# Kernel tuning notes

Hardware: AMD Instinct MI355X
Metric: run time of the kernel (lower is better)

Reference implementation:

```python
import jax, jax.numpy as jnp
import numpy as np

HID = 512; HH = HID // 2; INP = 1; OUT = 1
INH = int(HID * 0.3); EXC = HID - INH            # 153 / 359
N = 3 * HH + 2 * HID + INP                       # 1793 total units
ALM_EXC_START = 3 * HH + HID                      # start of ALM excitatory block
T_CONST = 0.1; SIGMA_REC = 0.01
B, T = 128, 300


def _np_masks():
    rng = np.random.default_rng(0)
    n_zeros = int(np.ceil(0.9 * HH))
    sparse = np.ones((HH, HH), np.float32)
    for c in range(HH):
        sparse[rng.permutation(HH)[:n_zeros], c] = 0.0
    alm2str = np.concatenate([np.ones((HH, EXC), np.float32), np.zeros((HH, INH), np.float32)], 1)
    thal2d1 = np.concatenate([np.ones((HH // 2, HID), np.float32), np.zeros((HH // 2, HID), np.float32)], 0)
    alm2d1 = 1.0 - thal2d1
    iti2d1 = np.concatenate([np.ones((HH // 2, INP), np.float32), np.zeros((HH // 2, INP), np.float32)], 0)
    alm_sign = np.concatenate([np.ones(EXC, np.float32), -np.ones(INH, np.float32)])  # alm2alm_D diagonal
    return sparse, alm2str, thal2d1, alm2d1, iti2d1, alm_sign

_SPARSE, _ALM2STR, _THAL2D1M, _ALM2D1M, _ITI2D1M, _ALMSIGN = [jnp.asarray(a) for a in _np_masks()]


def _clip(w):
    return jnp.clip(w, 1e-10, 1.0)               # F.hardtanh(w, 1e-10, 1)


def _build_W(d12d1_w, d12d2_w, d22d1_w, d22d2_w, d22stn_w, d12thal_w, stn2thal_w,
             thal2alm_w, alm2alm_w, thal2d1_w, thal2d2_w, alm2d1_w, alm2d2_w,
             inp_w_d1, inp_w_d2):
    z_ss = jnp.zeros((HH, HH)); z_sl = jnp.zeros((HH, HID))
    z_ls = jnp.zeros((HID, HH)); z_ll = jnp.zeros((HID, HID))
    z_si = jnp.zeros((HH, INP)); z_li = jnp.zeros((HID, INP))
    # striatal recurrence: sparse_mask * hardtanh(w) @ (-I)
    d12d1 = -(_SPARSE * _clip(d12d1_w)); d12d2 = -(_SPARSE * _clip(d12d2_w))
    d22d1 = -(_SPARSE * _clip(d22d1_w)); d22d2 = -(_SPARSE * _clip(d22d2_w))
    row_d1 = jnp.concatenate([d12d1, d22d1, z_ss, _THAL2D1M * _clip(thal2d1_w),
                              _ALM2D1M * _ALM2STR * _clip(alm2d1_w), _ITI2D1M * _clip(inp_w_d1)], 1)
    row_d2 = jnp.concatenate([d12d2, d22d2, z_ss, _clip(thal2d2_w),
                              _ALM2STR * _clip(alm2d2_w), _clip(inp_w_d2)], 1)
    row_stn = jnp.concatenate([z_ss, _clip(d22stn_w), z_ss, z_sl, z_sl, z_si], 1)
    row_thal = jnp.concatenate([_clip(d12thal_w), z_ls, -_clip(stn2thal_w), z_ll, z_ll, z_li], 1)  # stn2thal @ (-I)
    row_alm = jnp.concatenate([z_ls, z_ls, z_ls, _clip(thal2alm_w),
                               _clip(alm2alm_w) * _ALMSIGN[None, :], z_li], 1)      # alm2alm @ D (Dale)
    row_iti = jnp.zeros((INP, N))
    return jnp.concatenate([row_d1, row_d2, row_stn, row_thal, row_alm, row_iti], 0)


def setup_inputs() -> dict:
    key = jax.random.key(0)
    ks = jax.random.split(key, 24)
    u = lambda k, s: jax.random.uniform(k, s, jnp.float32) * 0.01   # uniform(0, 0.01) init
    return {
        "inp": jax.random.uniform(ks[0], (B, T, INP), jnp.float32),
        "cue_inp": jax.random.uniform(ks[1], (B, T, INP), jnp.float32),
        "inhib_stim": jnp.zeros((B, T, N), jnp.float32),
        "hn": jax.random.uniform(ks[2], (1, B, N), jnp.float32),
        "xn": jax.random.uniform(ks[3], (1, B, N), jnp.float32),
        "noise": jax.random.normal(ks[4], (B, T, N), jnp.float32),
        "d12d1_w": u(ks[5], (HH, HH)), "d12d2_w": u(ks[6], (HH, HH)),
        "d22d1_w": u(ks[7], (HH, HH)), "d22d2_w": u(ks[8], (HH, HH)),
        "d22stn_w": u(ks[9], (HH, HH)), "d12thal_w": u(ks[10], (HID, HH)),
        "stn2thal_w": u(ks[11], (HID, HH)), "thal2alm_w": u(ks[12], (HID, HID)),
        "alm2alm_w": u(ks[13], (HID, HID)), "thal2d1_w": u(ks[14], (HH, HID)),
        "thal2d2_w": u(ks[15], (HH, HID)), "alm2d1_w": u(ks[16], (HH, HID)),
        "alm2d2_w": u(ks[17], (HH, HID)), "inp_w_d1": u(ks[18], (HH, INP)),
        "inp_w_d2": u(ks[19], (HH, INP)), "out_w_alm": u(ks[20], (OUT, EXC)),
    }


def reference(inp, cue_inp, inhib_stim, hn, xn, noise,
              d12d1_w, d12d2_w, d22d1_w, d22d2_w, d22stn_w, d12thal_w, stn2thal_w,
              thal2alm_w, alm2alm_w, thal2d1_w, thal2d2_w, alm2d1_w, alm2d2_w,
              inp_w_d1, inp_w_d2, out_w_alm):
    W = _build_W(d12d1_w, d12d2_w, d22d1_w, d22d2_w, d22stn_w, d12thal_w, stn2thal_w,
                 thal2alm_w, alm2alm_w, thal2d1_w, thal2d2_w, alm2d1_w, alm2d2_w,
                 inp_w_d1, inp_w_d2)
    # tonic current: 0.1 everywhere except ITI units
    tonic = jnp.concatenate([0.1 * jnp.ones(N - INP, jnp.float32), jnp.zeros(INP, jnp.float32)])
    seq = (inhib_stim.swapaxes(0, 1),                 # [T, B, N]
           (inp + cue_inp).swapaxes(0, 1),            # [T, B, INP] -> injected into ITI units
           noise.swapaxes(0, 1))                      # [T, B, N]

    def step(carry, s):
        x, h = carry
        inh_t, iti_t, noise_t = s
        drive = h @ W.T + tonic + inh_t + SIGMA_REC * noise_t
        drive = drive.at[:, N - INP:].add(iti_t)
        x = x + T_CONST * (-x + drive)
        h = jax.nn.relu(x)
        out = h[:, ALM_EXC_START:ALM_EXC_START + EXC] @ out_w_alm.T
        return (x, h), (h, x, out)

    (_, _), (hs, xs, outs) = jax.lax.scan(step, (xn[0], hn[0]), seq)
    return hs.swapaxes(0, 1), xs.swapaxes(0, 1), outs.swapaxes(0, 1)
```

## Files before the change

kernel.cpp:

```cpp
#include <hip/hip_runtime.h>
#include <stdint.h>
#include <string.h>

#define NREAL 1793
#define NPAD  1824
#define NROWP 1808
#define WSTR  1832
#define NBLK  113
#define NGRP  2
#define TSTEPS 300
#define BATCH 128
#define XS_OFF 68851200
#define OUT_OFF 137702400
#define LOFF (16 * WSTR)
#define LOSCALE 4096.0f
#define LOINV  2.44140625e-4f

#define ARR_IDX(g,s)  (((g) * 8 + (s)) * 32)
#define MID_IDX(g)    ((16 + (g)) * 32)
#define FLAG_IDX(g,s) ((18 + (g) * 8 + (s)) * 32)
#define STRIPE_SZ(s)  ((s) == 0 ? 15u : 14u)

typedef _Float16 half_t;
typedef __attribute__((ext_vector_type(8))) _Float16 half8;
typedef __attribute__((ext_vector_type(4))) float f32x4;
typedef __attribute__((ext_vector_type(4))) unsigned int uint4v;

__device__ __forceinline__ float clipw(float w) {
  return fminf(fmaxf(w, 1e-10f), 1.0f);
}

__device__ __forceinline__ void store_pack_llc(uint32_t* p, uint32_t v) {
  asm volatile("global_store_dword %0, %1, off sc0 sc1"
               :: "v"((unsigned long long)(uintptr_t)p), "v"(v)
               : "memory");
}

__global__ __launch_bounds__(256)
void build_w(const float* __restrict__ d12d1, const float* __restrict__ d12d2,
             const float* __restrict__ d22d1, const float* __restrict__ d22d2,
             const float* __restrict__ d22stn, const float* __restrict__ d12thal,
             const float* __restrict__ stn2thal, const float* __restrict__ thal2alm,
             const float* __restrict__ alm2alm, const float* __restrict__ thal2d1,
             const float* __restrict__ thal2d2, const float* __restrict__ alm2d1,
             const float* __restrict__ alm2d2, const float* __restrict__ inpw1,
             const float* __restrict__ inpw2, const unsigned int* __restrict__ mbits,
             half_t* __restrict__ W)
{
  int idx = blockIdx.x * 256 + threadIdx.x;
  if (idx >= NROWP * NPAD) return;
  int i = idx / NPAD, j = idx - (idx / NPAD) * NPAD;
  float v = 0.f;
  if (i < NREAL && j < NREAL) {
    if (i < 256) {
      if (j < 512) {
        int jj = j & 255;
        unsigned bit = (mbits[(i << 3) + (jj >> 5)] >> (jj & 31)) & 1u;
        float wv = (j < 256) ? d12d1[(i << 8) + jj] : d22d1[(i << 8) + jj];
        v = bit ? -clipw(wv) : 0.f;
      } else if (j < 768) {
      } else if (j < 1280) {
        if (i < 128) v = clipw(thal2d1[(i << 9) + (j - 768)]);
      } else if (j < 1792) {
        int jj = j - 1280;
        if (i >= 128 && jj < 359) v = clipw(alm2d1[(i << 9) + jj]);
      } else {
        if (i < 128) v = clipw(inpw1[i]);
      }
    } else if (i < 512) {
      int ii = i - 256;
      if (j < 512) {
        int jj = j & 255;
        unsigned bit = (mbits[(ii << 3) + (jj >> 5)] >> (jj & 31)) & 1u;
        float wv = (j < 256) ? d12d2[(ii << 8) + jj] : d22d2[(ii << 8) + jj];
        v = bit ? -clipw(wv) : 0.f;
      } else if (j < 768) {
      } else if (j < 1280) {
        v = clipw(thal2d2[(ii << 9) + (j - 768)]);
      } else if (j < 1792) {
        int jj = j - 1280;
        if (jj < 359) v = clipw(alm2d2[(ii << 9) + jj]);
      } else {
        v = clipw(inpw2[ii]);
      }
    } else if (i < 768) {
      int ii = i - 512;
      if (j >= 256 && j < 512) v = clipw(d22stn[(ii << 8) + (j - 256)]);
    } else if (i < 1280) {
      int ii = i - 768;
      if (j < 256) v = clipw(d12thal[(ii << 8) + j]);
      else if (j >= 512 && j < 768) v = -clipw(stn2thal[(ii << 8) + (j - 512)]);
    } else if (i < 1792) {
      int ii = i - 1280;
      if (j >= 768 && j < 1280) v = clipw(thal2alm[(ii << 9) + (j - 768)]);
      else if (j >= 1280) {
        int jj = j - 1280;
        v = clipw(alm2alm[(ii << 9) + jj]) * ((jj < 359) ? 1.f : -1.f);
      }
    }
  }
  half_t vh = (half_t)v;
  half_t vl = (half_t)((v - (float)vh) * LOSCALE);
  W[idx] = vh;
  W[(size_t)NROWP * NPAD + idx] = vl;
}

__global__ __launch_bounds__(256)
void init_h(const float* __restrict__ hn, uint32_t* __restrict__ hbuf)
{
  const size_t P4 = (size_t)BATCH * NPAD;
  int idx = blockIdx.x * 256 + threadIdx.x;
  if (idx >= BATCH * NPAD) return;
  int b = idx / NPAD, k = idx - b * NPAD;
  float v = (k < NREAL) ? hn[b * NREAL + k] : 0.f;
  half_t vh = (half_t)v;
  half_t vl = (half_t)((v - (float)vh) * LOSCALE);
  uint32_t hp = (uint32_t)(*(unsigned short*)&vh) |
                ((uint32_t)(*(unsigned short*)&vl) << 16);
  hbuf[idx]      = hp;
  hbuf[P4 + idx] = 0u;
}

__global__ __launch_bounds__(256)
void rnn_step_all(const half_t* __restrict__ Wg, uint32_t* __restrict__ hbuf,
                  unsigned int* __restrict__ cnt,
                  const float* __restrict__ inp, const float* __restrict__ cue,
                  const float* __restrict__ inhib, const float* __restrict__ noise,
                  const float* __restrict__ xn, const float* __restrict__ outw,
                  float* __restrict__ dout)
{
  __shared__ __align__(16) half_t Wl[2 * 16 * WSTR];
  const int tid = threadIdx.x;
  const int bid = blockIdx.x;
  const int g  = bid / NBLK;
  const int nb = bid - g * NBLK;
  const int r0 = nb * 16;
  const int bg = g * 64;
  const size_t P4 = (size_t)BATCH * NPAD;

  const int lane = tid & 63;
  const int w    = tid >> 6;
  const int n_i  = lane & 15;
  const int kq   = lane >> 4;
  const int row  = r0 + n_i;
  const bool valid = row < NREAL;
  const int b0 = bg + 16 * w + kq * 4;
  const int bA = bg + 16 * w + n_i;
  const int wl_b = n_i * WSTR + kq * 8;

  float inh[4], noi[4];
  #pragma unroll
  for (int r = 0; r < 4; ++r) {
    inh[r] = 0.f; noi[r] = 0.f;
    if (valid) {
      int ei = ((b0 + r) * TSTEPS) * NREAL + row;
      inh[r] = __builtin_nontemporal_load(&inhib[ei]);
      noi[r] = __builtin_nontemporal_load(&noise[ei]);
    }
  }

  for (int idx = tid; idx < 2 * 16 * (NPAD / 8); idx += 256) {
    int p   = idx / (16 * (NPAD / 8));
    int rem = idx - p * 16 * (NPAD / 8);
    int rr  = rem / (NPAD / 8);
    int cc  = (rem - rr * (NPAD / 8)) * 8;
    *(uint4v*)&Wl[p * LOFF + rr * WSTR + cc] =
        *(const uint4v*)&Wg[(size_t)p * NROWP * NPAD + (size_t)(r0 + rr) * NPAD + cc];
  }
  __syncthreads();

  int lo0=0,hi0=0,lo1=0,hi1=0,lo2=0,hi2=0;
  if (r0 < 128)       { lo0=0;  hi0=16; lo1=24; hi1=40; lo2=56; hi2=57; }
  else if (r0 < 256)  { lo0=0;  hi0=16; lo1=40; hi1=52; }
  else if (r0 < 512)  { lo0=0;  hi0=16; lo1=24; hi1=52; lo2=56; hi2=57; }
  else if (r0 < 768)  { lo0=8;  hi0=16; }
  else if (r0 < 1280) { lo0=0;  hi0=8;  lo1=16; hi1=24; }
  else if (r0 < 1792) { lo0=24; hi0=56; }

  float xr[4];
  #pragma unroll
  for (int r = 0; r < 4; ++r)
    xr[r] = valid ? xn[(size_t)(b0 + r) * NREAL + row] : 0.f;

  const float wout = (valid && row >= 1280 && row < 1639) ? outw[row - 1280] : 0.f;
  const float tonic = (valid && row < 1792) ? 0.1f : 0.f;
  const bool is_iti = (row == 1792);
  const bool do_out = (r0 >= 1280 && r0 < 1639);

  #pragma unroll 1
  for (int t = 0; t < TSTEPS; ++t) {
    const uint32_t* hr = hbuf + (size_t)(t & 1) * P4;
    uint32_t*       hw = hbuf + (size_t)((t & 1) ^ 1) * P4;

    float itv[4];
    #pragma unroll
    for (int r = 0; r < 4; ++r) {
      int bt = (b0 + r) * TSTEPS + t;
      itv[r] = is_iti ? (inp[bt] + cue[bt]) : 0.f;
    }

    const uint32_t* ap = hr + (size_t)bA * NPAD + kq * 8;
    f32x4 acc0 = {0.f, 0.f, 0.f, 0.f};
    f32x4 acc1 = {0.f, 0.f, 0.f, 0.f};
    f32x4 acc2 = {0.f, 0.f, 0.f, 0.f};

#define DO_CHUNK(kc) { \
      uint4v q0 = *(const uint4v*)(ap + (kc) * 32); \
      uint4v q1 = *(const uint4v*)(ap + (kc) * 32 + 4); \
      uint4v uh, ul; \
      uh.x = __builtin_amdgcn_perm(q0.y, q0.x, 0x05040100u); \
      uh.y = __builtin_amdgcn_perm(q0.w, q0.z, 0x05040100u); \
      uh.z = __builtin_amdgcn_perm(q1.y, q1.x, 0x05040100u); \
      uh.w = __builtin_amdgcn_perm(q1.w, q1.z, 0x05040100u); \
      ul.x = __builtin_amdgcn_perm(q0.y, q0.x, 0x07060302u); \
      ul.y = __builtin_amdgcn_perm(q0.w, q0.z, 0x07060302u); \
      ul.z = __builtin_amdgcn_perm(q1.y, q1.x, 0x07060302u); \
      ul.w = __builtin_amdgcn_perm(q1.w, q1.z, 0x07060302u); \
      union { uint4v u; half8 h; } ch, cl; \
      ch.u = uh; cl.u = ul; \
      half8 bvh = *(const half8*)&Wl[wl_b + (kc) * 32]; \
      half8 bvl = *(const half8*)&Wl[LOFF + wl_b + (kc) * 32]; \
      acc0 = __builtin_amdgcn_mfma_f32_16x16x32_f16(ch.h, bvh, acc0, 0, 0, 0); \
      acc1 = __builtin_amdgcn_mfma_f32_16x16x32_f16(ch.h, bvl, acc1, 0, 0, 0); \
      acc2 = __builtin_amdgcn_mfma_f32_16x16x32_f16(cl.h, bvh, acc2, 0, 0, 0); }

    #pragma unroll 8
    for (int kc = lo0; kc < hi0; ++kc) DO_CHUNK(kc)
    #pragma unroll 8
    for (int kc = lo1; kc < hi1; ++kc) DO_CHUNK(kc)
    #pragma unroll 8
    for (int kc = lo2; kc < hi2; ++kc) DO_CHUNK(kc)
#undef DO_CHUNK

    float op[4];
    #pragma unroll
    for (int r = 0; r < 4; ++r) {
      float drive = acc0[r] + LOINV * (acc1[r] + acc2[r])
                    + tonic + inh[r] + 0.01f * noi[r] + itv[r];
      float xv = xr[r] + 0.1f * (drive - xr[r]);
      float hv = fmaxf(xv, 0.f);
      xr[r] = xv;
      int bt = (b0 + r) * TSTEPS + t;
      if (valid) {
        int ei = bt * NREAL + row;
        __builtin_nontemporal_store(hv, &dout[ei]);
        __builtin_nontemporal_store(xv, &dout[XS_OFF + ei]);
      }
      half_t hh = (half_t)hv;
      half_t hl = (half_t)((hv - (float)hh) * LOSCALE);
      uint32_t hp = (uint32_t)(*(unsigned short*)&hh) |
                    ((uint32_t)(*(unsigned short*)&hl) << 16);
      store_pack_llc(&hw[(size_t)(b0 + r) * NPAD + row], hp);
      op[r] = hv * wout;
    }

    if (do_out) {
      #pragma unroll
      for (int r = 0; r < 4; ++r) {
        float v = op[r];
        v += __shfl_xor(v, 1); v += __shfl_xor(v, 2);
        v += __shfl_xor(v, 4); v += __shfl_xor(v, 8);
        if (n_i == 0) atomicAdd(&dout[OUT_OFF + (b0 + r) * TSTEPS + t], v);
      }
    }

    if (t + 1 < TSTEPS) {
      #pragma unroll
      for (int r = 0; r < 4; ++r) {
        if (valid) {
          int ei = ((b0 + r) * TSTEPS + (t + 1)) * NREAL + row;
          inh[r] = __builtin_nontemporal_load(&inhib[ei]);
          noi[r] = __builtin_nontemporal_load(&noise[ei]);
        }
      }
      asm volatile("s_waitcnt vmcnt(8)" ::: "memory");
      __builtin_amdgcn_s_barrier();
      if (tid == 0) {
        const int s = nb & 7;
        const unsigned epoch = (unsigned)(t + 1);
        unsigned old = atomicAdd(&cnt[ARR_IDX(g, s)], 1u);
        if (old == epoch * STRIPE_SZ(s) - 1u) {
          unsigned mo = atomicAdd(&cnt[MID_IDX(g)], 1u);
          if (mo == epoch * 8u - 1u) {
            #pragma unroll
            for (int f = 0; f < 8; ++f)
              __hip_atomic_store(&cnt[FLAG_IDX(g, f)], epoch,
                                 __ATOMIC_RELAXED, __HIP_MEMORY_SCOPE_AGENT);
          }
        }
        int spins = 0;
        while (__hip_atomic_load(&cnt[FLAG_IDX(g, s)], __ATOMIC_RELAXED,
                                 __HIP_MEMORY_SCOPE_AGENT) < epoch) {
          if (spins < 4) {
            __builtin_amdgcn_s_sleep(1);
          } else {
            __builtin_amdgcn_s_sleep(8);
          }
          ++spins;
        }
        __builtin_amdgcn_fence(__ATOMIC_ACQUIRE, "agent");
      }
      __builtin_amdgcn_s_barrier();
    }
  }
}

static void compute_sparse_mask(uint32_t* mb) {
  uint32_t pool[4];
  uint32_t hc = 0x43b0d7e5u;
  auto hashmix = [&hc](uint32_t value) -> uint32_t {
    value ^= hc; hc *= 0x931e8875u; value *= hc; value ^= value >> 16; return value;
  };
  auto mixf = [](uint32_t x, uint32_t y) -> uint32_t {
    uint32_t r = x * 0xca01f9ddu;
    r -= y * 0x4973f715u;
    r ^= r >> 16;
    return r;
  };
  for (int i = 0; i < 4; ++i) pool[i] = hashmix(0u);
  for (int s = 0; s < 4; ++s)
    for (int d = 0; d < 4; ++d)
      if (s != d) pool[d] = mixf(pool[d], hashmix(pool[s]));
  uint32_t st[8];
  uint32_t hb = 0x8b51f9ddu;
  for (int i = 0; i < 8; ++i) {
    uint32_t dv = pool[i & 3];
    dv ^= hb; hb *= 0x58f38dedu; dv *= hb; dv ^= dv >> 16;
    st[i] = dv;
  }
  uint64_t v64[4];
  for (int i = 0; i < 4; ++i) v64[i] = (uint64_t)st[2 * i] | ((uint64_t)st[2 * i + 1] << 32);
  typedef unsigned __int128 u128;
  const u128 MULT = ((u128)0x2360ed051fc65da4ULL << 64) | 0x4385df649fccf645ULL;
  u128 initstate = ((u128)v64[0] << 64) | v64[1];
  u128 initseq   = ((u128)v64[2] << 64) | v64[3];
  u128 state = 0, inc = (initseq << 1) | 1;
  state = state * MULT + inc;
  state += initstate;
  state = state * MULT + inc;
  bool has32 = false; uint32_t cached = 0;
  auto next64 = [&]() -> uint64_t {
    state = state * MULT + inc;
    uint64_t hi = (uint64_t)(state >> 64), lo = (uint64_t)state;
    unsigned rot = (unsigned)(state >> 122);
    uint64_t x = hi ^ lo;
    return (x >> rot) | (x << ((64 - rot) & 63));
  };
  auto next32 = [&]() -> uint32_t {
    if (has32) { has32 = false; return cached; }
    uint64_t v = next64();
    has32 = true; cached = (uint32_t)(v >> 32);
    return (uint32_t)v;
  };
  auto rinterval = [&](uint32_t mx) -> uint32_t {
    if (mx == 0) return 0;
    uint32_t mask = mx;
    mask |= mask >> 1; mask |= mask >> 2; mask |= mask >> 4;
    mask |= mask >> 8; mask |= mask >> 16;
    uint32_t value;
    do { value = next32() & mask; } while (value > mx);
    return value;
  };
  for (int i = 0; i < 256 * 8; ++i) mb[i] = 0xFFFFFFFFu;
  int perm[256];
  for (int c = 0; c < 256; ++c) {
    for (int i = 0; i < 256; ++i) perm[i] = i;
    for (int i = 255; i >= 1; --i) {
      uint32_t j = rinterval((uint32_t)i);
      int tmp = perm[i]; perm[i] = perm[j]; perm[j] = tmp;
    }
    for (int z = 0; z < 231; ++z)
      mb[perm[z] * 8 + (c >> 5)] &= ~(1u << (c & 31));
  }
}

extern "C" void kernel_launch(void* const* d_in, const int* in_sizes, int n_in,
                              void* d_out, int out_size, void* d_ws, size_t ws_size,
                              hipStream_t stream)
{
  (void)in_sizes; (void)n_in; (void)out_size; (void)ws_size;
  const float* inp   = (const float*)d_in[0];
  const float* cue   = (const float*)d_in[1];
  const float* inhib = (const float*)d_in[2];
  const float* hn    = (const float*)d_in[3];
  const float* xn    = (const float*)d_in[4];
  const float* noise = (const float*)d_in[5];
  const float* outw  = (const float*)d_in[21];
  float* dout = (float*)d_out;

  char* ws = (char*)d_ws;
  const size_t W_BYTES = (size_t)2 * NROWP * NPAD * sizeof(half_t);
  const size_t H_BYTES = (size_t)2 * BATCH * NPAD * 4;
  half_t*   W    = (half_t*)ws;
  uint32_t* hbuf = (uint32_t*)(ws + W_BYTES);
  unsigned int* mbits = (unsigned int*)(ws + W_BYTES + H_BYTES);
  unsigned int* cnt   = (unsigned int*)(ws + W_BYTES + H_BYTES + 8192);

  static uint32_t hmask[256 * 8];
  compute_sparse_mask(hmask);
  (void)hipMemcpyAsync(mbits, hmask, sizeof(hmask), hipMemcpyHostToDevice, stream);
  (void)hipMemsetAsync(cnt, 0, 8192, stream);
  (void)hipMemsetAsync((char*)d_out + (size_t)OUT_OFF * 4, 0, 38400 * 4, stream);

  build_w<<<(NROWP * NPAD + 255) / 256, 256, 0, stream>>>(
      (const float*)d_in[6],  (const float*)d_in[7],  (const float*)d_in[8],
      (const float*)d_in[9],  (const float*)d_in[10], (const float*)d_in[11],
      (const float*)d_in[12], (const float*)d_in[13], (const float*)d_in[14],
      (const float*)d_in[15], (const float*)d_in[16], (const float*)d_in[17],
      (const float*)d_in[18], (const float*)d_in[19], (const float*)d_in[20],
      mbits, W);
  init_h<<<(BATCH * NPAD + 255) / 256, 256, 0, stream>>>(hn, hbuf);

  void* args[] = {(void*)&W, (void*)&hbuf, (void*)&cnt, (void*)&inp, (void*)&cue,
                  (void*)&inhib, (void*)&noise, (void*)&xn, (void*)&outw, (void*)&dout};
  hipError_t err = hipLaunchCooperativeKernel(reinterpret_cast<void*>(rnn_step_all),
                                              dim3(NGRP * NBLK), dim3(256), args, 0, stream);
  if (err != hipSuccess) {
    rnn_step_all<<<dim3(NGRP * NBLK), dim3(256), 0, stream>>>(
        W, hbuf, cnt, inp, cue, inhib, noise, xn, outw, dout);
  }
}
```

Measured before the change: 4.808 ms.

## Move output projection to a single block one step late and batch h loads

```diff
diff --git a/kernel.cpp b/kernel.cpp
--- a/kernel.cpp
+++ b/kernel.cpp
@@ -34,6 +34,54 @@
   asm volatile("global_store_dword %0, %1, off sc0 sc1"
                :: "v"((unsigned long long)(uintptr_t)p), "v"(v)
                : "memory");
+}
+
+__device__ __forceinline__ float unpack_h(uint32_t p) {
+  unsigned short uh = (unsigned short)(p & 0xffffu);
+  unsigned short ul = (unsigned short)(p >> 16);
+  half_t hh = *(half_t*)&uh;
+  half_t hl = *(half_t*)&ul;
+  return (float)hh + LOINV * (float)hl;
+}
+
+template<int LO0, int N0, int LO1, int N1, int LO2, int N2>
+__device__ __forceinline__ void seg_mfma(const uint32_t* __restrict__ ap,
+                                         const half_t* __restrict__ Wl, int wl_b,
+                                         f32x4& acc0, f32x4& acc1, f32x4& acc2)
+{
+  constexpr int NC = N0 + N1 + N2;
+  if (NC == 0) return;
+  uint4v q0[NC ? NC : 1], q1[NC ? NC : 1];
+  #pragma unroll
+  for (int i = 0; i < NC; ++i) {
+    const int kc = (i < N0) ? (LO0 + i)
+                 : (i < N0 + N1) ? (LO1 + i - N0)
+                 : (LO2 + i - N0 - N1);
+    q0[i] = *(const uint4v*)(ap + kc * 32);
+    q1[i] = *(const uint4v*)(ap + kc * 32 + 4);
+  }
+  #pragma unroll
+  for (int i = 0; i < NC; ++i) {
+    const int kc = (i < N0) ? (LO0 + i)
+                 : (i < N0 + N1) ? (LO1 + i - N0)
+                 : (LO2 + i - N0 - N1);
+    uint4v uh, ul;
+    uh.x = __builtin_amdgcn_perm(q0[i].y, q0[i].x, 0x05040100u);
+    uh.y = __builtin_amdgcn_perm(q0[i].w, q0[i].z, 0x05040100u);
+    uh.z = __builtin_amdgcn_perm(q1[i].y, q1[i].x, 0x05040100u);
+    uh.w = __builtin_amdgcn_perm(q1[i].w, q1[i].z, 0x05040100u);
+    ul.x = __builtin_amdgcn_perm(q0[i].y, q0[i].x, 0x07060302u);
+    ul.y = __builtin_amdgcn_perm(q0[i].w, q0[i].z, 0x07060302u);
+    ul.z = __builtin_amdgcn_perm(q1[i].y, q1[i].x, 0x07060302u);
+    ul.w = __builtin_amdgcn_perm(q1[i].w, q1[i].z, 0x07060302u);
+    union { uint4v u; half8 h; } ch, cl;
+    ch.u = uh; cl.u = ul;
+    half8 bvh = *(const half8*)&Wl[wl_b + kc * 32];
+    half8 bvl = *(const half8*)&Wl[LOFF + wl_b + kc * 32];
+    acc0 = __builtin_amdgcn_mfma_f32_16x16x32_f16(ch.h, bvh, acc0, 0, 0, 0);
+    acc1 = __builtin_amdgcn_mfma_f32_16x16x32_f16(ch.h, bvl, acc1, 0, 0, 0);
+    acc2 = __builtin_amdgcn_mfma_f32_16x16x32_f16(cl.h, bvh, acc2, 0, 0, 0);
+  }
 }
 
 __global__ __launch_bounds__(256)
@@ -121,7 +169,7 @@
   hbuf[P4 + idx] = 0u;
 }
 
-__global__ __launch_bounds__(256)
+__global__ __launch_bounds__(256, 1)
 void rnn_step_all(const half_t* __restrict__ Wg, uint32_t* __restrict__ hbuf,
                   unsigned int* __restrict__ cnt,
                   const float* __restrict__ inp, const float* __restrict__ cue,
@@ -147,6 +195,7 @@
   const int b0 = bg + 16 * w + kq * 4;
   const int bA = bg + 16 * w + n_i;
   const int wl_b = n_i * WSTR + kq * 8;
+  const bool is_outblk = (r0 == 512);
 
   float inh[4], noi[4];
   #pragma unroll
@@ -169,23 +218,18 @@
   }
   __syncthreads();
 
-  int lo0=0,hi0=0,lo1=0,hi1=0,lo2=0,hi2=0;
-  if (r0 < 128)       { lo0=0;  hi0=16; lo1=24; hi1=40; lo2=56; hi2=57; }
-  else if (r0 < 256)  { lo0=0;  hi0=16; lo1=40; hi1=52; }
-  else if (r0 < 512)  { lo0=0;  hi0=16; lo1=24; hi1=52; lo2=56; hi2=57; }
-  else if (r0 < 768)  { lo0=8;  hi0=16; }
-  else if (r0 < 1280) { lo0=0;  hi0=8;  lo1=16; hi1=24; }
-  else if (r0 < 1792) { lo0=24; hi0=56; }
-
   float xr[4];
   #pragma unroll
   for (int r = 0; r < 4; ++r)
     xr[r] = valid ? xn[(size_t)(b0 + r) * NREAL + row] : 0.f;
 
-  const float wout = (valid && row >= 1280 && row < 1639) ? outw[row - 1280] : 0.f;
   const float tonic = (valid && row < 1792) ? 0.1f : 0.f;
   const bool is_iti = (row == 1792);
-  const bool do_out = (r0 >= 1280 && r0 < 1639);
+
+  const int ob    = bg + 16 * w + (lane >> 2);
+  const int opart = lane & 3;
+  const int ou0   = opart * 90;
+  const int onu   = (opart == 3) ? 89 : 90;
 
   #pragma unroll 1
   for (int t = 0; t < TSTEPS; ++t) {
@@ -204,35 +248,13 @@
     f32x4 acc1 = {0.f, 0.f, 0.f, 0.f};
     f32x4 acc2 = {0.f, 0.f, 0.f, 0.f};
 
-#define DO_CHUNK(kc) { \
-      uint4v q0 = *(const uint4v*)(ap + (kc) * 32); \
-      uint4v q1 = *(const uint4v*)(ap + (kc) * 32 + 4); \
-      uint4v uh, ul; \
-      uh.x = __builtin_amdgcn_perm(q0.y, q0.x, 0x05040100u); \
-      uh.y = __builtin_amdgcn_perm(q0.w, q0.z, 0x05040100u); \
-      uh.z = __builtin_amdgcn_perm(q1.y, q1.x, 0x05040100u); \
-      uh.w = __builtin_amdgcn_perm(q1.w, q1.z, 0x05040100u); \
-      ul.x = __builtin_amdgcn_perm(q0.y, q0.x, 0x07060302u); \
-      ul.y = __builtin_amdgcn_perm(q0.w, q0.z, 0x07060302u); \
-      ul.z = __builtin_amdgcn_perm(q1.y, q1.x, 0x07060302u); \
-      ul.w = __builtin_amdgcn_perm(q1.w, q1.z, 0x07060302u); \
-      union { uint4v u; half8 h; } ch, cl; \
-      ch.u = uh; cl.u = ul; \
-      half8 bvh = *(const half8*)&Wl[wl_b + (kc) * 32]; \
-      half8 bvl = *(const half8*)&Wl[LOFF + wl_b + (kc) * 32]; \
-      acc0 = __builtin_amdgcn_mfma_f32_16x16x32_f16(ch.h, bvh, acc0, 0, 0, 0); \
-      acc1 = __builtin_amdgcn_mfma_f32_16x16x32_f16(ch.h, bvl, acc1, 0, 0, 0); \
-      acc2 = __builtin_amdgcn_mfma_f32_16x16x32_f16(cl.h, bvh, acc2, 0, 0, 0); }
-
-    #pragma unroll 8
-    for (int kc = lo0; kc < hi0; ++kc) DO_CHUNK(kc)
-    #pragma unroll 8
-    for (int kc = lo1; kc < hi1; ++kc) DO_CHUNK(kc)
-    #pragma unroll 8
-    for (int kc = lo2; kc < hi2; ++kc) DO_CHUNK(kc)
-#undef DO_CHUNK
-
-    float op[4];
+    if      (r0 < 128)  seg_mfma<0, 16, 24, 16, 56, 1>(ap, Wl, wl_b, acc0, acc1, acc2);
+    else if (r0 < 256)  seg_mfma<0, 16, 40, 12,  0, 0>(ap, Wl, wl_b, acc0, acc1, acc2);
+    else if (r0 < 512)  seg_mfma<0, 16, 24, 28, 56, 1>(ap, Wl, wl_b, acc0, acc1, acc2);
+    else if (r0 < 768)  seg_mfma<8,  8,  0,  0,  0, 0>(ap, Wl, wl_b, acc0, acc1, acc2);
+    else if (r0 < 1280) seg_mfma<0,  8, 16,  8,  0, 0>(ap, Wl, wl_b, acc0, acc1, acc2);
+    else if (r0 < 1792) seg_mfma<24, 32, 0,  0,  0, 0>(ap, Wl, wl_b, acc0, acc1, acc2);
+
     #pragma unroll
     for (int r = 0; r < 4; ++r) {
       float drive = acc0[r] + LOINV * (acc1[r] + acc2[r])
@@ -251,17 +273,18 @@
       uint32_t hp = (uint32_t)(*(unsigned short*)&hh) |
                     ((uint32_t)(*(unsigned short*)&hl) << 16);
       store_pack_llc(&hw[(size_t)(b0 + r) * NPAD + row], hp);
-      op[r] = hv * wout;
-    }
-
-    if (do_out) {
-      #pragma unroll
-      for (int r = 0; r < 4; ++r) {
-        float v = op[r];
-        v += __shfl_xor(v, 1); v += __shfl_xor(v, 2);
-        v += __shfl_xor(v, 4); v += __shfl_xor(v, 8);
-        if (n_i == 0) atomicAdd(&dout[OUT_OFF + (b0 + r) * TSTEPS + t], v);
-      }
+    }
+
+    if (is_outblk && t >= 1) {
+      const uint32_t* hb = hr + (size_t)ob * NPAD + 1280 + ou0;
+      float s = 0.f;
+      #pragma unroll 10
+      for (int i = 0; i < onu; ++i)
+        s += unpack_h(hb[i]) * outw[ou0 + i];
+      s += __shfl_xor(s, 1);
+      s += __shfl_xor(s, 2);
+      if (opart == 0)
+        __builtin_nontemporal_store(s, &dout[OUT_OFF + ob * TSTEPS + (t - 1)]);
     }
 
     if (t + 1 < TSTEPS) {
@@ -302,6 +325,50 @@
       }
       __builtin_amdgcn_s_barrier();
     }
+  }
+
+  asm volatile("s_waitcnt vmcnt(0)" ::: "memory");
+  __builtin_amdgcn_s_barrier();
+  if (tid == 0) {
+    const int s = nb & 7;
+    const unsigned epoch = (unsigned)TSTEPS;
+    unsigned old = atomicAdd(&cnt[ARR_IDX(g, s)], 1u);
+    if (old == epoch * STRIPE_SZ(s) - 1u) {
+      unsigned mo = atomicAdd(&cnt[MID_IDX(g)], 1u);
+      if (mo == epoch * 8u - 1u) {
+        #pragma unroll
+        for (int f = 0; f < 8; ++f)
+          __hip_atomic_store(&cnt[FLAG_IDX(g, f)], epoch,
+                             __ATOMIC_RELAXED, __HIP_MEMORY_SCOPE_AGENT);
+      }
+    }
+  }
+  if (is_outblk) {
+    if (tid == 0) {
+      const int s = nb & 7;
+      int spins = 0;
+      while (__hip_atomic_load(&cnt[FLAG_IDX(g, s)], __ATOMIC_RELAXED,
+                               __HIP_MEMORY_SCOPE_AGENT) < (unsigned)TSTEPS) {
+        if (spins < 4) {
+          __builtin_amdgcn_s_sleep(1);
+        } else {
+          __builtin_amdgcn_s_sleep(8);
+        }
+        ++spins;
+      }
+      __builtin_amdgcn_fence(__ATOMIC_ACQUIRE, "agent");
+    }
+    __builtin_amdgcn_s_barrier();
+    const uint32_t* hr = hbuf + (size_t)(TSTEPS & 1) * P4;
+    const uint32_t* hb = hr + (size_t)ob * NPAD + 1280 + ou0;
+    float s = 0.f;
+    #pragma unroll 10
+    for (int i = 0; i < onu; ++i)
+      s += unpack_h(hb[i]) * outw[ou0 + i];
+    s += __shfl_xor(s, 1);
+    s += __shfl_xor(s, 2);
+    if (opart == 0)
+      __builtin_nontemporal_store(s, &dout[OUT_OFF + ob * TSTEPS + (TSTEPS - 1)]);
   }
 }
 
@@ -400,7 +467,6 @@
   compute_sparse_mask(hmask);
   (void)hipMemcpyAsync(mbits, hmask, sizeof(hmask), hipMemcpyHostToDevice, stream);
   (void)hipMemsetAsync(cnt, 0, 8192, stream);
-  (void)hipMemsetAsync((char*)d_out + (size_t)OUT_OFF * 4, 0, 38400 * 4, stream);
 
   build_w<<<(NROWP * NPAD + 255) / 256, 256, 0, stream>>>(
       (const float*)d_in[6],  (const float*)d_in[7],  (const float*)d_in[8],
```

Measured after the change: 4.177 ms. 13.1% less time.
